# Optimization experiments

Hardware: AMD Instinct MI355X
Metric: run time of the kernel (lower is better)

The kernel has to match this reference:

```python
import jax, jax.numpy as jnp
import numpy as np

B, Q, H, W = 64, 300, 40, 40  # batch, num_queries, feature-map H,W (img/32)


def setup_inputs() -> dict:
    key = jax.random.key(0)
    k1, k2, k3 = jax.random.split(key, 3)
    obj_coord = jax.random.uniform(k1, (B, Q, 4), dtype=jnp.float32)  # sigmoid cxcywh
    sub_coord = jax.random.uniform(k2, (B, Q, 4), dtype=jnp.float32)
    img_size = jax.random.randint(k3, (B, 2), 800, 1280, dtype=jnp.int64)  # (h, w)
    mask = jnp.zeros((B, H, W), dtype=bool)  # only its shape is used
    return {"obj_coord": obj_coord, "sub_coord": sub_coord, "img_size": img_size, "mask": mask}


def _box_cxcywh_to_xyxy(b):
    cx, cy, w, h = b[..., 0], b[..., 1], b[..., 2], b[..., 3]
    return cx - 0.5 * w, cy - 0.5 * h, cx + 0.5 * w, cy + 0.5 * h


def _mask_from_query(coord, img_size, Hm, Wm):
    # coord: [B,Q,4] cxcywh in [0,1]; img_size: [B,2] = (img_h, img_w)
    x1, y1, x2, y2 = _box_cxcywh_to_xyxy(coord)
    sw = img_size[:, 1:2].astype(jnp.float32)  # [B,1]
    sh = img_size[:, 0:1].astype(jnp.float32)
    # torch: (coord * size) // 32 then .long()  (floor division on floats == floor)
    x1 = jnp.floor(x1 * sw / 32.0).astype(jnp.int32)
    y1 = jnp.floor(y1 * sh / 32.0).astype(jnp.int32)
    x2 = jnp.floor(x2 * sw / 32.0).astype(jnp.int32)
    y2 = jnp.floor(y2 * sh / 32.0).astype(jnp.int32)
    x2 = jnp.minimum(x2, Wm - 1)
    y2 = jnp.minimum(y2, Hm - 1)
    hh = jnp.arange(Hm, dtype=jnp.int32)[:, None]  # [H,1]
    ww = jnp.arange(Wm, dtype=jnp.int32)[None, :]  # [1,W]
    # True OUTSIDE the (inclusive) box: single fused broadcast compare, [B,Q,H,W]
    return ((hh < y1[..., None, None]) | (hh > y2[..., None, None]) |
            (ww < x1[..., None, None]) | (ww > x2[..., None, None]))


def reference(obj_coord, sub_coord, img_size, mask):
    Hm, Wm = mask.shape[1], mask.shape[2]
    mask_object = _mask_from_query(obj_coord, img_size, Hm, Wm)
    mask_human = _mask_from_query(sub_coord, img_size, Hm, Wm)
    # stack object/human masks; float32 so fwd and fwdbwd share output structure
    return jnp.stack([mask_object, mask_human], axis=0).astype(jnp.float32)
```

## Files before the change

kernel.cpp:

```cpp
#include <hip/hip_runtime.h>


#define B_ 64
#define Q_ 300
#define HM 40
#define WM 40

#define N4 15360000

__global__ __launch_bounds__(256) void partmap_kernel(
    const float* __restrict__ obj,
    const float* __restrict__ sub,
    const int*   __restrict__ img,
    float4*      __restrict__ out)
{
    #pragma clang fp contract(off)

    int idx = blockIdx.x * 256 + threadIdx.x;

    int w4  = idx % 10;
    int t   = idx / 10;
    int h   = t % HM;
    int sbq = t / HM;
    int q   = sbq % Q_;
    int sb  = sbq / Q_;
    int b   = sb & 63;
    int s   = sb >> 6;

    const float* coord = s ? sub : obj;
    float4 c = ((const float4*)coord)[b * Q_ + q];

    float sh = (float)img[b * 2 + 0];
    float sw = (float)img[b * 2 + 1];

    float x1f = (c.x - 0.5f * c.z) * sw / 32.0f;
    float y1f = (c.y - 0.5f * c.w) * sh / 32.0f;
    float x2f = (c.x + 0.5f * c.z) * sw / 32.0f;
    float y2f = (c.y + 0.5f * c.w) * sh / 32.0f;

    int x1 = (int)floorf(x1f);
    int y1 = (int)floorf(y1f);
    int x2 = (int)floorf(x2f);
    int y2 = (int)floorf(y2f);
    x2 = min(x2, WM - 1);
    y2 = min(y2, HM - 1);

    bool rowout = (h < y1) || (h > y2);
    int w0 = w4 * 4;

    float4 r;
    r.x = (rowout || (w0     < x1) || (w0     > x2)) ? 1.0f : 0.0f;
    r.y = (rowout || (w0 + 1 < x1) || (w0 + 1 > x2)) ? 1.0f : 0.0f;
    r.z = (rowout || (w0 + 2 < x1) || (w0 + 2 > x2)) ? 1.0f : 0.0f;
    r.w = (rowout || (w0 + 3 < x1) || (w0 + 3 > x2)) ? 1.0f : 0.0f;

    out[idx] = r;
}

extern "C" void kernel_launch(void* const* d_in, const int* in_sizes, int n_in,
                              void* d_out, int out_size, void* d_ws, size_t ws_size,
                              hipStream_t stream) {
    const float* obj = (const float*)d_in[0];
    const float* sub = (const float*)d_in[1];
    const int*   img = (const int*)d_in[2];

    float4* out = (float4*)d_out;

    dim3 grid(N4 / 256);
    dim3 block(256);
    partmap_kernel<<<grid, block, 0, stream>>>(obj, sub, img, out);
}
```

Measured before the change: 261.8 us.

## Precompute per-box bitmask table and stream float4 masks from it

Splits the work into two kernels. A small prep kernel computes each box's bounds once and packs a 40-bit column-outside mask plus the row bounds y1/y2 into a two-word table in workspace. The main kernel then builds each float4 from a shift, a sign-based row test and bit extraction. This removes the per-element float box math and some integer division, at the cost of an extra launch and a dependent table read.

```diff
diff --git a/kernel.cpp b/kernel.cpp
--- a/kernel.cpp
+++ b/kernel.cpp
@@ -1,31 +1,28 @@
 #include <hip/hip_runtime.h>
+#include <stdint.h>
 
 
 #define B_ 64
 #define Q_ 300
 #define HM 40
 #define WM 40
+#define NBOX (2 * B_ * Q_)
+#define N4   15360000
 
-#define N4 15360000
-
-__global__ __launch_bounds__(256) void partmap_kernel(
+__global__ __launch_bounds__(256) void box_prep_kernel(
     const float* __restrict__ obj,
     const float* __restrict__ sub,
     const int*   __restrict__ img,
-    float4*      __restrict__ out)
+    uint32_t*    __restrict__ tbl)
 {
     #pragma clang fp contract(off)
+    int id = blockIdx.x * 256 + threadIdx.x;
+    if (id >= NBOX) return;
 
-    int idx = blockIdx.x * 256 + threadIdx.x;
-
-    int w4  = idx % 10;
-    int t   = idx / 10;
-    int h   = t % HM;
-    int sbq = t / HM;
-    int q   = sbq % Q_;
-    int sb  = sbq / Q_;
-    int b   = sb & 63;
-    int s   = sb >> 6;
+    int q  = id % Q_;
+    int sb = id / Q_;
+    int b  = sb & 63;
+    int s  = sb >> 6;
 
     const float* coord = s ? sub : obj;
     float4 c = ((const float4*)coord)[b * Q_ + q];
@@ -40,19 +37,50 @@
 
     int x1 = (int)floorf(x1f);
     int y1 = (int)floorf(y1f);
-    int x2 = (int)floorf(x2f);
-    int y2 = (int)floorf(y2f);
-    x2 = min(x2, WM - 1);
-    y2 = min(y2, HM - 1);
+    int x2 = min((int)floorf(x2f), WM - 1);
+    int y2 = min((int)floorf(y2f), HM - 1);
 
-    bool rowout = (h < y1) || (h > y2);
+    uint64_t lo = (x1 <= 0) ? ~0ull : ~((1ull << x1) - 1ull);
+    uint64_t hi = (1ull << (x2 + 1)) - 1ull;
+    uint64_t outside = (~(lo & hi)) & ((1ull << 40) - 1ull);
+
+    uint32_t d0 = (uint32_t)outside;
+    uint32_t d1 = ((uint32_t)(outside >> 32) & 0xFFu)
+                | (((uint32_t)y1 & 0xFFu) << 8)
+                | (((uint32_t)y2 & 0xFFu) << 16);
+
+    tbl[id * 2 + 0] = d0;
+    tbl[id * 2 + 1] = d1;
+}
+
+__global__ __launch_bounds__(256) void partmap_stream_kernel(
+    const uint32_t* __restrict__ tbl,
+    float4*         __restrict__ out)
+{
+    int idx = blockIdx.x * 256 + threadIdx.x;
+
+    int sbq = idx / 400;
+    int rem = idx - sbq * 400;
+    int h   = rem / 10;
+    int w4  = rem - h * 10;
+
+    uint32_t d0 = tbl[sbq * 2 + 0];
+    uint32_t d1 = tbl[sbq * 2 + 1];
+
+    int y1 = (int)(int8_t)(d1 >> 8);
+    int y2 = (int)(int8_t)(d1 >> 16);
+
+    int rneg = ((h - y1) | (y2 - h)) >> 31;
+
     int w0 = w4 * 4;
+    uint32_t shifted = (uint32_t)((((uint64_t)d1 << 32) | d0) >> w0);
+    uint32_t m = shifted | (uint32_t)rneg;
 
     float4 r;
-    r.x = (rowout || (w0     < x1) || (w0     > x2)) ? 1.0f : 0.0f;
-    r.y = (rowout || (w0 + 1 < x1) || (w0 + 1 > x2)) ? 1.0f : 0.0f;
-    r.z = (rowout || (w0 + 2 < x1) || (w0 + 2 > x2)) ? 1.0f : 0.0f;
-    r.w = (rowout || (w0 + 3 < x1) || (w0 + 3 > x2)) ? 1.0f : 0.0f;
+    r.x = (float)( m        & 1u);
+    r.y = (float)((m >> 1)  & 1u);
+    r.z = (float)((m >> 2)  & 1u);
+    r.w = (float)((m >> 3)  & 1u);
 
     out[idx] = r;
 }
@@ -64,9 +92,9 @@
     const float* sub = (const float*)d_in[1];
     const int*   img = (const int*)d_in[2];
 
-    float4* out = (float4*)d_out;
+    uint32_t* tbl = (uint32_t*)d_ws;
+    float4*   out = (float4*)d_out;
 
-    dim3 grid(N4 / 256);
-    dim3 block(256);
-    partmap_kernel<<<grid, block, 0, stream>>>(obj, sub, img, out);
+    box_prep_kernel<<<dim3((NBOX + 255) / 256), dim3(256), 0, stream>>>(obj, sub, img, tbl);
+    partmap_stream_kernel<<<dim3(N4 / 256), dim3(256), 0, stream>>>(tbl, out);
 }
```

Result: faster. 235.1 us (-10.2%).

## Compute each box once per wave and broadcast bitmask via readlane

Applied to the files above, without the earlier changes.

Restructures the kernel so each wavefront handles four boxes: box bounds are computed once per box, converted to a 40-bit column-outside mask, and broadcast to all lanes with readlane. Each lane then writes seven float4 rows per box using cheap shifts and a row-check sign trick. This removes per-element index division and redundant coordinate loads and floor math, leaving the kernel closer to pure store bandwidth. It relies on 64-bit shifts staying in range for the given coordinate domain.

```diff
diff --git a/kernel.cpp b/kernel.cpp
--- a/kernel.cpp
+++ b/kernel.cpp
@@ -1,60 +1,88 @@
 #include <hip/hip_runtime.h>
+#include <stdint.h>
 
 
-#define B_ 64
-#define Q_ 300
-#define HM 40
-#define WM 40
+#define B_   64
+#define Q_   300
+#define HM   40
+#define WM   40
+#define NBOX 38400
+#define EPW  4
 
-#define N4 15360000
-
-__global__ __launch_bounds__(256) void partmap_kernel(
+__global__ __launch_bounds__(256) void partmap_fused(
     const float* __restrict__ obj,
     const float* __restrict__ sub,
     const int*   __restrict__ img,
     float4*      __restrict__ out)
 {
     #pragma clang fp contract(off)
+    const int tid  = threadIdx.x;
+    const int lane = tid & 63;
+    const int wid  = (blockIdx.x << 2) | (tid >> 6);
+    const int e0   = wid * EPW;
 
-    int idx = blockIdx.x * 256 + threadIdx.x;
+    int h_j[7], sh_j[7];
+    #pragma unroll
+    for (int j = 0; j < 7; ++j) {
+        int p  = j * 64 + lane;
+        int h  = p / 10;
+        int w4 = p - 10 * h;
+        h_j[j]  = h;
+        sh_j[j] = w4 * 4;
+    }
 
-    int w4  = idx % 10;
-    int t   = idx / 10;
-    int h   = t % HM;
-    int sbq = t / HM;
-    int q   = sbq % Q_;
-    int sb  = sbq / Q_;
-    int b   = sb & 63;
-    int s   = sb >> 6;
+    int id = e0 + (lane & 3);
+    int q  = id % Q_;
+    int sb = id / Q_;
+    int b  = sb & 63;
+    int s  = sb >> 6;
 
     const float* coord = s ? sub : obj;
     float4 c = ((const float4*)coord)[b * Q_ + q];
 
-    float sh = (float)img[b * 2 + 0];
-    float sw = (float)img[b * 2 + 1];
+    float shh = (float)img[b * 2 + 0];
+    float sww = (float)img[b * 2 + 1];
 
-    float x1f = (c.x - 0.5f * c.z) * sw / 32.0f;
-    float y1f = (c.y - 0.5f * c.w) * sh / 32.0f;
-    float x2f = (c.x + 0.5f * c.z) * sw / 32.0f;
-    float y2f = (c.y + 0.5f * c.w) * sh / 32.0f;
+    float x1f = (c.x - 0.5f * c.z) * sww / 32.0f;
+    float y1f = (c.y - 0.5f * c.w) * shh / 32.0f;
+    float x2f = (c.x + 0.5f * c.z) * sww / 32.0f;
+    float y2f = (c.y + 0.5f * c.w) * shh / 32.0f;
 
     int x1 = (int)floorf(x1f);
     int y1 = (int)floorf(y1f);
-    int x2 = (int)floorf(x2f);
-    int y2 = (int)floorf(y2f);
-    x2 = min(x2, WM - 1);
-    y2 = min(y2, HM - 1);
+    int x2 = min((int)floorf(x2f), WM - 1);
+    int y2 = min((int)floorf(y2f), HM - 1);
 
-    bool rowout = (h < y1) || (h > y2);
-    int w0 = w4 * 4;
+    uint64_t blo = (x1 <= 0) ? ~0ull : ~((1ull << x1) - 1ull);
+    uint64_t bhi = (1ull << (x2 + 1)) - 1ull;
+    uint64_t outside = (~(blo & bhi)) & ((1ull << 40) - 1ull);
+    uint32_t d0 = (uint32_t)outside;
+    uint32_t d1 = (uint32_t)(outside >> 32);
 
-    float4 r;
-    r.x = (rowout || (w0     < x1) || (w0     > x2)) ? 1.0f : 0.0f;
-    r.y = (rowout || (w0 + 1 < x1) || (w0 + 1 > x2)) ? 1.0f : 0.0f;
-    r.z = (rowout || (w0 + 2 < x1) || (w0 + 2 > x2)) ? 1.0f : 0.0f;
-    r.w = (rowout || (w0 + 3 < x1) || (w0 + 3 > x2)) ? 1.0f : 0.0f;
+    float4* bp = out + (size_t)e0 * 400 + lane;
 
-    out[idx] = r;
+    #pragma unroll
+    for (int e = 0; e < EPW; ++e) {
+        uint32_t sd0 = (uint32_t)__builtin_amdgcn_readlane((int)d0, e);
+        uint32_t sd1 = (uint32_t)__builtin_amdgcn_readlane((int)d1, e);
+        int      sy1 = __builtin_amdgcn_readlane(y1, e);
+        int      sy2 = __builtin_amdgcn_readlane(y2, e);
+        uint64_t m64 = ((uint64_t)sd1 << 32) | (uint64_t)sd0;
+        float4*  ep  = bp + e * 400;
+
+        #pragma unroll
+        for (int j = 0; j < 7; ++j) {
+            int rneg = ((h_j[j] - sy1) | (sy2 - h_j[j])) >> 31;
+            uint32_t m = (uint32_t)(m64 >> sh_j[j]) | (uint32_t)rneg;
+            float4 r;
+            r.x = (float)( m        & 1u);
+            r.y = (float)((m >> 1u) & 1u);
+            r.z = (float)((m >> 2u) & 1u);
+            r.w = (float)((m >> 3u) & 1u);
+            if (j < 6 || lane < 16)
+                ep[j * 64] = r;
+        }
+    }
 }
 
 extern "C" void kernel_launch(void* const* d_in, const int* in_sizes, int n_in,
@@ -66,7 +94,5 @@
 
     float4* out = (float4*)d_out;
 
-    dim3 grid(N4 / 256);
-    dim3 block(256);
-    partmap_kernel<<<grid, block, 0, stream>>>(obj, sub, img, out);
+    partmap_fused<<<dim3(NBOX / (EPW * 4)), dim3(256), 0, stream>>>(obj, sub, img, out);
 }
```

New measurement: 240.6 us. 1.09x faster.
